# Optimization experiments

Measured on AMD Instinct MI355X. Metric: run time of the kernel, lower is better.

## Reference

```python
import jax, jax.numpy as jnp
import numpy as np

GAMMA = 2.5
K = 4
RHO = 0.085
TAU_CLIP = 5.0
NUM_HEADS = 8


def setup_inputs() -> dict:
    key = jax.random.key(0)
    ks = jax.random.split(key, 4)
    B, T, C = 2, 2048, 512
    x = jax.random.normal(ks[0], (B, T, C), jnp.float32)
    tau = jax.random.uniform(ks[1], (B, T, T), jnp.float32)
    s = 1.0 / np.sqrt(C)
    Wqkv = jax.random.normal(ks[2], (C, 3 * C), jnp.float32) * s
    bqkv = jnp.zeros((3 * C,), jnp.float32)
    Wproj = jax.random.normal(ks[3], (C, C), jnp.float32) * s
    bproj = jnp.zeros((C,), jnp.float32)
    return dict(x=x, tau=tau, Wqkv=Wqkv, bqkv=bqkv, Wproj=Wproj, bproj=bproj)


def reference(x, tau, Wqkv, bqkv, Wproj, bproj):
    B, T, C = x.shape
    H = NUM_HEADS
    D = C // H
    qkv = x @ Wqkv + bqkv                       # [B,T,3C]
    q, k, v = jnp.split(qkv, 3, axis=-1)
    q = q.reshape(B, T, H, D).transpose(0, 2, 1, 3)   # [B,H,T,D]
    k = k.reshape(B, T, H, D).transpose(0, 2, 1, 3)
    v = v.reshape(B, T, H, D).transpose(0, 2, 1, 3)
    scale = D ** -0.5
    logits = jnp.einsum('bhtd,bhsd->bhts', q, k) * scale   # [B,H,T,T]
    pheromone_bias = GAMMA * jnp.log(tau + 1e-8)           # [B,T,T]
    logits = logits + pheromone_bias[:, None]
    # top-K keys per query from tau define the sparse mask (LOCAL_WINDOW=0)
    k_val = min(K, T)
    idx = jax.lax.top_k(tau, k_val)[1]                     # [B,T,K]
    mask = jnp.zeros((B, T, T), bool).at[
        jnp.arange(B)[:, None, None], jnp.arange(T)[None, :, None], idx
    ].set(True)
    logits = jnp.where(mask[:, None], logits, -jnp.inf)
    attn = jax.nn.softmax(logits, axis=-1)                 # [B,H,T,T]
    # EMA pheromone (tau) update, no gradient in original (torch.no_grad)
    signal = attn.mean(axis=1)                             # [B,T,T]
    tau_new = (1.0 - RHO) * tau + signal ** 3
    tau_new = tau_new / (tau_new.sum(axis=-1, keepdims=True) + 1e-8)
    tau_new = jnp.minimum(tau_new, TAU_CLIP)
    tau_new = jax.lax.stop_gradient(tau_new)
    out = jnp.einsum('bhts,bhsd->bthd', attn, v).reshape(B, T, C)
    out = out @ Wproj + bproj
    return out, tau_new
```

## Files before the change

### kernel.cpp

```cpp
#include <hip/hip_runtime.h>
#include <hip/hip_bf16.h>
#include <math.h>

#define BB 2
#define TT 2048
#define CC 512
#define HH 8
#define DD 64
#define KK 4
#define C3 1536
#define MROWS (BB*TT)

#define G1_NT (C3/64)
#define G1_BLOCKS (G1_NT*(MROWS/128))
#define G2_NT (CC/64)
#define G2_BLOCKS (G2_NT*(MROWS/128))

typedef __attribute__((ext_vector_type(8))) short bf16x8;
typedef __attribute__((ext_vector_type(4))) float floatx4;

static __device__ __forceinline__ unsigned short f2bf(float f) {
  unsigned int u = __float_as_uint(f);
  return (unsigned short)((u + 0x7fffu + ((u >> 16) & 1u)) >> 16);
}
static __device__ __forceinline__ float bf2f(unsigned short u) {
  return __uint_as_float(((unsigned int)u) << 16);
}

template<bool BF16OUT>
static __device__ __forceinline__ void gemm_body(
    int bid, int nt,
    const unsigned short* __restrict__ A,
    const unsigned short* __restrict__ Bt,
    const float* __restrict__ bias,
    void* __restrict__ Cout, int N, int K) {
  __shared__ bf16x8 As[128 * 4];
  __shared__ bf16x8 Bs[64 * 4];
  const int tid  = threadIdx.x;
  const int wave = tid >> 6;
  const int lane = tid & 63;
  const int n0 = (bid % nt) * 64;
  const int m0 = (bid / nt) * 128;
  const int m_off = (wave >> 1) * 64;
  const int n_off = (wave & 1) * 32;
  const int lrow = lane >> 2;
  const int lx   = ((lane & 3) ^ ((lane >> 3) & 3)) * 8;
  const int fr = lane & 15;
  const int fq = lane >> 4;
  const int key = (fr >> 1) & 3;

  floatx4 acc[4][2];
#pragma unroll
  for (int i = 0; i < 4; ++i)
#pragma unroll
    for (int j = 0; j < 2; ++j) acc[i][j] = (floatx4){0.f, 0.f, 0.f, 0.f};

  for (int k0 = 0; k0 < K; k0 += 32) {
#pragma unroll
    for (int s = 0; s < 2; ++s) {
      int q = wave * 2 + s;
      const unsigned short* ga = A + (size_t)(m0 + q * 16 + lrow) * K + k0 + lx;
      __builtin_amdgcn_global_load_lds(
          (const __attribute__((address_space(1))) void*)ga,
          (__attribute__((address_space(3))) void*)((char*)As + q * 1024), 16, 0, 0);
    }
    const unsigned short* gb = Bt + (size_t)(n0 + wave * 16 + lrow) * K + k0 + lx;
    __builtin_amdgcn_global_load_lds(
        (const __attribute__((address_space(1))) void*)gb,
        (__attribute__((address_space(3))) void*)((char*)Bs + wave * 1024), 16, 0, 0);
    __syncthreads();
    bf16x8 a[4], b[2];
#pragma unroll
    for (int i = 0; i < 4; ++i)
      a[i] = As[(m_off + i * 16 + fr) * 4 + (fq ^ key)];
#pragma unroll
    for (int j = 0; j < 2; ++j)
      b[j] = Bs[(n_off + j * 16 + fr) * 4 + (fq ^ key)];
#pragma unroll
    for (int i = 0; i < 4; ++i)
#pragma unroll
      for (int j = 0; j < 2; ++j)
        acc[i][j] = __builtin_amdgcn_mfma_f32_16x16x32_bf16(a[i], b[j], acc[i][j], 0, 0, 0);
    __syncthreads();
  }
#pragma unroll
  for (int j = 0; j < 2; ++j) {
    int col = n0 + n_off + j * 16 + fr;
    float bv = bias[col];
#pragma unroll
    for (int i = 0; i < 4; ++i) {
#pragma unroll
      for (int r = 0; r < 4; ++r) {
        int row = m0 + m_off + i * 16 + fq * 4 + r;
        float v = acc[i][j][r] + bv;
        if (BF16OUT) ((unsigned short*)Cout)[(size_t)row * N + col] = f2bf(v);
        else         ((float*)Cout)[(size_t)row * N + col] = v;
      }
    }
  }
}

static __device__ __forceinline__ bool kv_better(float av, int ai, float bv, int bi) {
  return av > bv || (av == bv && ai < bi);
}
static __device__ __forceinline__ void kv_ce(float* v, int* i, int a, int b) {
  if (!kv_better(v[a], i[a], v[b], i[b])) {
    float tv = v[a]; v[a] = v[b]; v[b] = tv;
    int   ti = i[a]; i[a] = i[b]; i[b] = ti;
  }
}
static __device__ __forceinline__ void kv_merge(
    float* av, int* ai, const float* bv, const int* bi) {
  float cv[4]; int ci[4];
#pragma unroll
  for (int j = 0; j < 4; ++j) {
    bool t = kv_better(av[j], ai[j], bv[3 - j], bi[3 - j]);
    cv[j] = t ? av[j] : bv[3 - j];
    ci[j] = t ? ai[j] : bi[3 - j];
  }
  kv_ce(cv, ci, 0, 2); kv_ce(cv, ci, 1, 3);
  kv_ce(cv, ci, 0, 1); kv_ce(cv, ci, 2, 3);
#pragma unroll
  for (int j = 0; j < 4; ++j) { av[j] = cv[j]; ai[j] = ci[j]; }
}

static __device__ __forceinline__ void topk_body(
    int row, const float* __restrict__ tau, int* __restrict__ idx_out) {
  const int tid = threadIdx.x;
  const float4* rp = (const float4*)(tau + (size_t)row * TT);
  float4 f0 = rp[tid * 2], f1 = rp[tid * 2 + 1];
  float e[8] = { f0.x, f0.y, f0.z, f0.w, f1.x, f1.y, f1.z, f1.w };
  const int base = tid * 8;

  float tv[4] = { -1e30f, -1e30f, -1e30f, -1e30f };
  int   ti[4] = { 1 << 30, 1 << 30, 1 << 30, 1 << 30 };
#pragma unroll
  for (int k = 0; k < 8; ++k) {
    float v = e[k];
    if (v > tv[3]) {
      tv[3] = v; ti[3] = base + k;
      if (tv[3] > tv[2]) { float a=tv[2]; tv[2]=tv[3]; tv[3]=a; int b=ti[2]; ti[2]=ti[3]; ti[3]=b; }
      if (tv[2] > tv[1]) { float a=tv[1]; tv[1]=tv[2]; tv[2]=a; int b=ti[1]; ti[1]=ti[2]; ti[2]=b; }
      if (tv[1] > tv[0]) { float a=tv[0]; tv[0]=tv[1]; tv[1]=a; int b=ti[0]; ti[0]=ti[1]; ti[1]=b; }
    }
  }

#pragma unroll
  for (int step = 1; step <= 32; step <<= 1) {
    float bv[4]; int bi[4];
#pragma unroll
    for (int j = 0; j < 4; ++j) {
      bv[j] = __shfl_xor(tv[j], step, 64);
      bi[j] = __shfl_xor(ti[j], step, 64);
    }
    kv_merge(tv, ti, bv, bi);
  }

  __shared__ float swv[4][4];
  __shared__ int   swi[4][4];
  const int wave = tid >> 6, lane = tid & 63;
  if (lane == 0) {
#pragma unroll
    for (int j = 0; j < 4; ++j) { swv[wave][j] = tv[j]; swi[wave][j] = ti[j]; }
  }
  __syncthreads();
  if (tid == 0) {
    float m0[4], m1[4]; int x0[4], x1[4];
#pragma unroll
    for (int j = 0; j < 4; ++j) { m0[j] = swv[0][j]; x0[j] = swi[0][j]; }
#pragma unroll
    for (int j = 0; j < 4; ++j) { m1[j] = swv[1][j]; x1[j] = swi[1][j]; }
    kv_merge(m0, x0, m1, x1);
#pragma unroll
    for (int j = 0; j < 4; ++j) { m1[j] = swv[2][j]; x1[j] = swi[2][j]; }
    float m2[4]; int x2[4];
#pragma unroll
    for (int j = 0; j < 4; ++j) { m2[j] = swv[3][j]; x2[j] = swi[3][j]; }
    kv_merge(m1, x1, m2, x2);
    kv_merge(m0, x0, m1, x1);
    int4 w = { x0[0], x0[1], x0[2], x0[3] };
    *((int4*)(idx_out + row * KK)) = w;
  }
}

static __device__ __forceinline__ void transpose_body(
    int t, int nbx, const float* __restrict__ W, unsigned short* __restrict__ Wt,
    int R, int Cn) {
  __shared__ unsigned short tile[32][33];
  const int c0 = (t % nbx) * 32, r0 = (t / nbx) * 32;
  const int tx = threadIdx.x & 31, ty = threadIdx.x >> 5;
#pragma unroll
  for (int i = 0; i < 4; ++i) {
    int r = ty + i * 8;
    tile[r][tx] = f2bf(W[(size_t)(r0 + r) * Cn + c0 + tx]);
  }
  __syncthreads();
#pragma unroll
  for (int i = 0; i < 4; ++i) {
    int r = ty + i * 8;
    Wt[(size_t)(c0 + r) * R + r0 + tx] = tile[tx][r];
  }
}

__global__ __launch_bounds__(256) void prep_kernel(
    const float* __restrict__ x, unsigned short* __restrict__ x_bf,
    const float* __restrict__ Wqkv, unsigned short* __restrict__ wqkv_t,
    const float* __restrict__ Wproj, unsigned short* __restrict__ wproj_t) {
  const int bid = blockIdx.x;
  if (bid < 1024) {
    int g = bid * 256 + threadIdx.x;
    const float4* p = (const float4*)x;
    float4 f0 = p[g * 2], f1 = p[g * 2 + 1];
    union { unsigned short u[8]; uint4 v; } pk;
    pk.u[0]=f2bf(f0.x); pk.u[1]=f2bf(f0.y); pk.u[2]=f2bf(f0.z); pk.u[3]=f2bf(f0.w);
    pk.u[4]=f2bf(f1.x); pk.u[5]=f2bf(f1.y); pk.u[6]=f2bf(f1.z); pk.u[7]=f2bf(f1.w);
    ((uint4*)x_bf)[g] = pk.v;
  } else if (bid < 1024 + 768) {
    transpose_body(bid - 1024, C3 / 32, Wqkv, wqkv_t, CC, C3);
  } else {
    transpose_body(bid - 1792, CC / 32, Wproj, wproj_t, CC, CC);
  }
}

__global__ __launch_bounds__(256) void gemm1_topk_kernel(
    const unsigned short* __restrict__ x_bf,
    const unsigned short* __restrict__ wqkv_t,
    const float* __restrict__ bqkv, unsigned short* __restrict__ qkv_bf,
    const float* __restrict__ tau, int* __restrict__ idx_out) {
  if (blockIdx.x < G1_BLOCKS)
    gemm_body<true>(blockIdx.x, G1_NT, x_bf, wqkv_t, bqkv, qkv_bf, C3, CC);
  else
    topk_body(blockIdx.x - G1_BLOCKS, tau, idx_out);
}

__global__ __launch_bounds__(512) void attn_tau_kernel(
    const unsigned short* __restrict__ qkv, const float* __restrict__ tau,
    const int* __restrict__ idx_in, unsigned short* __restrict__ attn_bf,
    float* __restrict__ tau_out) {
  const int row  = blockIdx.x;
  const int b    = row >> 11;
  const int tid  = threadIdx.x;
  const int h    = tid >> 6;
  const int lane = tid & 63;

  __shared__ int   idx4[KK];
  __shared__ float tau4[KK];
  __shared__ float ps[HH][KK];
  __shared__ float s3s[KK];
  if (tid < KK) {
    int s = idx_in[row * KK + tid];
    idx4[tid] = s;
    tau4[tid] = tau[(size_t)row * TT + s];
  }
  const float4* rp = (const float4*)(tau + (size_t)row * TT);
  float4 tv4 = rp[tid];
  __syncthreads();

  const float q = bf2f(qkv[(size_t)row * C3 + h * DD + lane]);
  float kv[KK], vv[KK];
#pragma unroll
  for (int j = 0; j < KK; ++j) {
    size_t bs = ((size_t)(b * TT + idx4[j])) * C3 + h * DD + lane;
    kv[j] = bf2f(qkv[bs + CC]);
    vv[j] = bf2f(qkv[bs + 2 * CC]);
  }

  float p[KK];
#pragma unroll
  for (int j = 0; j < KK; ++j) p[j] = q * kv[j];
#pragma unroll
  for (int off = 32; off > 0; off >>= 1)
#pragma unroll
    for (int j = 0; j < KK; ++j) p[j] += __shfl_xor(p[j], off, 64);

  float logit[KK];
#pragma unroll
  for (int j = 0; j < KK; ++j)
    logit[j] = p[j] * 0.125f + 2.5f * logf(tau4[j] + 1e-8f);

  float m = fmaxf(fmaxf(logit[0], logit[1]), fmaxf(logit[2], logit[3]));
  float den = 0.f;
#pragma unroll
  for (int j = 0; j < KK; ++j) { p[j] = expf(logit[j] - m); den += p[j]; }
  float inv = 1.f / den;
#pragma unroll
  for (int j = 0; j < KK; ++j) p[j] *= inv;

  float o = 0.f;
#pragma unroll
  for (int j = 0; j < KK; ++j) o += p[j] * vv[j];
  attn_bf[(size_t)row * CC + h * DD + lane] = f2bf(o);

  if (lane < KK) ps[h][lane] = p[lane];
  __syncthreads();
  if (tid < KK) {
    float s = 0.f;
#pragma unroll
    for (int k = 0; k < HH; ++k) s += ps[k][tid];
    s *= (1.0f / HH);
    s3s[tid] = s * s * s;
  }
  __syncthreads();

  float v[4] = { tv4.x, tv4.y, tv4.z, tv4.w };
  int i4[KK]; float s3[KK];
#pragma unroll
  for (int j = 0; j < KK; ++j) { i4[j] = idx4[j]; s3[j] = s3s[j]; }
  const float keep = 1.0f - 0.085f;
  const int base = tid * 4;
  float local = 0.f;
#pragma unroll
  for (int i = 0; i < 4; ++i) {
    float t = keep * v[i];
#pragma unroll
    for (int j = 0; j < KK; ++j)
      if (base + i == i4[j]) t += s3[j];
    v[i] = t;
    local += t;
  }
#pragma unroll
  for (int off = 32; off > 0; off >>= 1) local += __shfl_xor(local, off, 64);
  __shared__ float wsum[HH];
  __shared__ float tot;
  if (lane == 0) wsum[h] = local;
  __syncthreads();
  if (tid == 0) {
    float s = 0.f;
#pragma unroll
    for (int k = 0; k < HH; ++k) s += wsum[k];
    tot = s;
  }
  __syncthreads();
  float invs = 1.f / (tot + 1e-8f);
  float4 o4 = { fminf(v[0]*invs,5.f), fminf(v[1]*invs,5.f),
                fminf(v[2]*invs,5.f), fminf(v[3]*invs,5.f) };
  ((float4*)(tau_out + (size_t)row * TT))[tid] = o4;
}

__global__ __launch_bounds__(256) void gemm2_kernel(
    const unsigned short* __restrict__ attn_bf,
    const unsigned short* __restrict__ wproj_t,
    const float* __restrict__ bproj, float* __restrict__ out) {
  gemm_body<false>(blockIdx.x, G2_NT, attn_bf, wproj_t, bproj, out, CC, CC);
}

extern "C" void kernel_launch(void* const* d_in, const int* in_sizes, int n_in,
                              void* d_out, int out_size, void* d_ws, size_t ws_size,
                              hipStream_t stream) {
  const float* x     = (const float*)d_in[0];
  const float* tau   = (const float*)d_in[1];
  const float* Wqkv  = (const float*)d_in[2];
  const float* bqkv  = (const float*)d_in[3];
  const float* Wproj = (const float*)d_in[4];
  const float* bproj = (const float*)d_in[5];

  float* out     = (float*)d_out;
  float* tau_new = out + (size_t)MROWS * CC;

  char* w = (char*)d_ws;
  unsigned short* qkv_bf  = (unsigned short*)w; w += (size_t)MROWS * C3 * 2;
  unsigned short* x_bf    = (unsigned short*)w; w += (size_t)MROWS * CC * 2;
  unsigned short* wqkv_t  = (unsigned short*)w; w += (size_t)C3 * CC * 2;
  unsigned short* wproj_t = (unsigned short*)w; w += (size_t)CC * CC * 2;
  unsigned short* attn_bf = (unsigned short*)w; w += (size_t)MROWS * CC * 2;
  int*   idx = (int*)w;

  prep_kernel<<<2048, 256, 0, stream>>>(x, x_bf, Wqkv, wqkv_t, Wproj, wproj_t);

  gemm1_topk_kernel<<<G1_BLOCKS + MROWS, 256, 0, stream>>>(
      x_bf, wqkv_t, bqkv, qkv_bf, tau, idx);

  attn_tau_kernel<<<MROWS, 512, 0, stream>>>(qkv_bf, tau, idx, attn_bf, tau_new);

  gemm2_kernel<<<G2_BLOCKS, 256, 0, stream>>>(attn_bf, wproj_t, bproj, out);
}
```

Measured before the change: 145.7 us.

## Fuse top-k selection into attention/tau row kernel to read tau once

Moves the per-row top-k over tau out of the gemm1 kernel and into the per-row attention/tau-update kernel, which now holds the tau row in registers for both top-k and the EMA normalization. This removes a second full read of tau and the index buffer round trip. The row kernel drops to 256 threads with each wave handling two heads, and top-k no longer overlaps with the QKV GEMM.

```diff
diff --git a/kernel.cpp b/kernel.cpp
--- a/kernel.cpp
+++ b/kernel.cpp
@@ -124,65 +124,6 @@
   for (int j = 0; j < 4; ++j) { av[j] = cv[j]; ai[j] = ci[j]; }
 }
 
-static __device__ __forceinline__ void topk_body(
-    int row, const float* __restrict__ tau, int* __restrict__ idx_out) {
-  const int tid = threadIdx.x;
-  const float4* rp = (const float4*)(tau + (size_t)row * TT);
-  float4 f0 = rp[tid * 2], f1 = rp[tid * 2 + 1];
-  float e[8] = { f0.x, f0.y, f0.z, f0.w, f1.x, f1.y, f1.z, f1.w };
-  const int base = tid * 8;
-
-  float tv[4] = { -1e30f, -1e30f, -1e30f, -1e30f };
-  int   ti[4] = { 1 << 30, 1 << 30, 1 << 30, 1 << 30 };
-#pragma unroll
-  for (int k = 0; k < 8; ++k) {
-    float v = e[k];
-    if (v > tv[3]) {
-      tv[3] = v; ti[3] = base + k;
-      if (tv[3] > tv[2]) { float a=tv[2]; tv[2]=tv[3]; tv[3]=a; int b=ti[2]; ti[2]=ti[3]; ti[3]=b; }
-      if (tv[2] > tv[1]) { float a=tv[1]; tv[1]=tv[2]; tv[2]=a; int b=ti[1]; ti[1]=ti[2]; ti[2]=b; }
-      if (tv[1] > tv[0]) { float a=tv[0]; tv[0]=tv[1]; tv[1]=a; int b=ti[0]; ti[0]=ti[1]; ti[1]=b; }
-    }
-  }
-
-#pragma unroll
-  for (int step = 1; step <= 32; step <<= 1) {
-    float bv[4]; int bi[4];
-#pragma unroll
-    for (int j = 0; j < 4; ++j) {
-      bv[j] = __shfl_xor(tv[j], step, 64);
-      bi[j] = __shfl_xor(ti[j], step, 64);
-    }
-    kv_merge(tv, ti, bv, bi);
-  }
-
-  __shared__ float swv[4][4];
-  __shared__ int   swi[4][4];
-  const int wave = tid >> 6, lane = tid & 63;
-  if (lane == 0) {
-#pragma unroll
-    for (int j = 0; j < 4; ++j) { swv[wave][j] = tv[j]; swi[wave][j] = ti[j]; }
-  }
-  __syncthreads();
-  if (tid == 0) {
-    float m0[4], m1[4]; int x0[4], x1[4];
-#pragma unroll
-    for (int j = 0; j < 4; ++j) { m0[j] = swv[0][j]; x0[j] = swi[0][j]; }
-#pragma unroll
-    for (int j = 0; j < 4; ++j) { m1[j] = swv[1][j]; x1[j] = swi[1][j]; }
-    kv_merge(m0, x0, m1, x1);
-#pragma unroll
-    for (int j = 0; j < 4; ++j) { m1[j] = swv[2][j]; x1[j] = swi[2][j]; }
-    float m2[4]; int x2[4];
-#pragma unroll
-    for (int j = 0; j < 4; ++j) { m2[j] = swv[3][j]; x2[j] = swi[3][j]; }
-    kv_merge(m1, x1, m2, x2);
-    kv_merge(m0, x0, m1, x1);
-    int4 w = { x0[0], x0[1], x0[2], x0[3] };
-    *((int4*)(idx_out + row * KK)) = w;
-  }
-}
-
 static __device__ __forceinline__ void transpose_body(
     int t, int nbx, const float* __restrict__ W, unsigned short* __restrict__ Wt,
     int R, int Cn) {
@@ -222,76 +163,121 @@
   }
 }
 
-__global__ __launch_bounds__(256) void gemm1_topk_kernel(
+__global__ __launch_bounds__(256) void gemm1_kernel(
     const unsigned short* __restrict__ x_bf,
     const unsigned short* __restrict__ wqkv_t,
-    const float* __restrict__ bqkv, unsigned short* __restrict__ qkv_bf,
-    const float* __restrict__ tau, int* __restrict__ idx_out) {
-  if (blockIdx.x < G1_BLOCKS)
-    gemm_body<true>(blockIdx.x, G1_NT, x_bf, wqkv_t, bqkv, qkv_bf, C3, CC);
-  else
-    topk_body(blockIdx.x - G1_BLOCKS, tau, idx_out);
-}
-
-__global__ __launch_bounds__(512) void attn_tau_kernel(
+    const float* __restrict__ bqkv, unsigned short* __restrict__ qkv_bf) {
+  gemm_body<true>(blockIdx.x, G1_NT, x_bf, wqkv_t, bqkv, qkv_bf, C3, CC);
+}
+
+__global__ __launch_bounds__(256) void row_kernel(
     const unsigned short* __restrict__ qkv, const float* __restrict__ tau,
-    const int* __restrict__ idx_in, unsigned short* __restrict__ attn_bf,
-    float* __restrict__ tau_out) {
+    unsigned short* __restrict__ attn_bf, float* __restrict__ tau_out) {
   const int row  = blockIdx.x;
   const int b    = row >> 11;
   const int tid  = threadIdx.x;
-  const int h    = tid >> 6;
+  const int wv   = tid >> 6;
   const int lane = tid & 63;
 
   __shared__ int   idx4[KK];
   __shared__ float tau4[KK];
   __shared__ float ps[HH][KK];
   __shared__ float s3s[KK];
-  if (tid < KK) {
-    int s = idx_in[row * KK + tid];
-    idx4[tid] = s;
-    tau4[tid] = tau[(size_t)row * TT + s];
-  }
+  __shared__ float swv[4][4];
+  __shared__ int   swi[4][4];
+  __shared__ float wsum[4];
+  __shared__ float tot;
+
   const float4* rp = (const float4*)(tau + (size_t)row * TT);
-  float4 tv4 = rp[tid];
-  __syncthreads();
-
-  const float q = bf2f(qkv[(size_t)row * C3 + h * DD + lane]);
-  float kv[KK], vv[KK];
-#pragma unroll
-  for (int j = 0; j < KK; ++j) {
-    size_t bs = ((size_t)(b * TT + idx4[j])) * C3 + h * DD + lane;
-    kv[j] = bf2f(qkv[bs + CC]);
-    vv[j] = bf2f(qkv[bs + 2 * CC]);
-  }
-
-  float p[KK];
-#pragma unroll
-  for (int j = 0; j < KK; ++j) p[j] = q * kv[j];
-#pragma unroll
-  for (int off = 32; off > 0; off >>= 1)
-#pragma unroll
-    for (int j = 0; j < KK; ++j) p[j] += __shfl_xor(p[j], off, 64);
-
-  float logit[KK];
-#pragma unroll
-  for (int j = 0; j < KK; ++j)
-    logit[j] = p[j] * 0.125f + 2.5f * logf(tau4[j] + 1e-8f);
-
-  float m = fmaxf(fmaxf(logit[0], logit[1]), fmaxf(logit[2], logit[3]));
-  float den = 0.f;
-#pragma unroll
-  for (int j = 0; j < KK; ++j) { p[j] = expf(logit[j] - m); den += p[j]; }
-  float inv = 1.f / den;
-#pragma unroll
-  for (int j = 0; j < KK; ++j) p[j] *= inv;
-
-  float o = 0.f;
-#pragma unroll
-  for (int j = 0; j < KK; ++j) o += p[j] * vv[j];
-  attn_bf[(size_t)row * CC + h * DD + lane] = f2bf(o);
-
-  if (lane < KK) ps[h][lane] = p[lane];
+  float4 f0 = rp[tid * 2], f1 = rp[tid * 2 + 1];
+  float e[8] = { f0.x, f0.y, f0.z, f0.w, f1.x, f1.y, f1.z, f1.w };
+  const int base = tid * 8;
+
+  float tv[4] = { -1e30f, -1e30f, -1e30f, -1e30f };
+  int   ti[4] = { 1 << 30, 1 << 30, 1 << 30, 1 << 30 };
+#pragma unroll
+  for (int k = 0; k < 8; ++k) {
+    float v = e[k];
+    if (v > tv[3]) {
+      tv[3] = v; ti[3] = base + k;
+      if (tv[3] > tv[2]) { float a=tv[2]; tv[2]=tv[3]; tv[3]=a; int c=ti[2]; ti[2]=ti[3]; ti[3]=c; }
+      if (tv[2] > tv[1]) { float a=tv[1]; tv[1]=tv[2]; tv[2]=a; int c=ti[1]; ti[1]=ti[2]; ti[2]=c; }
+      if (tv[1] > tv[0]) { float a=tv[0]; tv[0]=tv[1]; tv[1]=a; int c=ti[0]; ti[0]=ti[1]; ti[1]=c; }
+    }
+  }
+#pragma unroll
+  for (int step = 1; step <= 32; step <<= 1) {
+    float bv[4]; int bi[4];
+#pragma unroll
+    for (int j = 0; j < 4; ++j) {
+      bv[j] = __shfl_xor(tv[j], step, 64);
+      bi[j] = __shfl_xor(ti[j], step, 64);
+    }
+    kv_merge(tv, ti, bv, bi);
+  }
+  if (lane == 0) {
+#pragma unroll
+    for (int j = 0; j < 4; ++j) { swv[wv][j] = tv[j]; swi[wv][j] = ti[j]; }
+  }
+  __syncthreads();
+  if (tid == 0) {
+    float m0[4], m1[4]; int x0[4], x1[4];
+#pragma unroll
+    for (int j = 0; j < 4; ++j) { m0[j] = swv[0][j]; x0[j] = swi[0][j]; }
+#pragma unroll
+    for (int j = 0; j < 4; ++j) { m1[j] = swv[1][j]; x1[j] = swi[1][j]; }
+    kv_merge(m0, x0, m1, x1);
+#pragma unroll
+    for (int j = 0; j < 4; ++j) { m1[j] = swv[2][j]; x1[j] = swi[2][j]; }
+    float m2[4]; int x2[4];
+#pragma unroll
+    for (int j = 0; j < 4; ++j) { m2[j] = swv[3][j]; x2[j] = swi[3][j]; }
+    kv_merge(m1, x1, m2, x2);
+    kv_merge(m0, x0, m1, x1);
+#pragma unroll
+    for (int j = 0; j < 4; ++j) { idx4[j] = x0[j]; tau4[j] = m0[j]; }
+  }
+  __syncthreads();
+
+  int   i4[KK]; float t4[KK];
+#pragma unroll
+  for (int j = 0; j < KK; ++j) { i4[j] = idx4[j]; t4[j] = tau4[j]; }
+
+#pragma unroll
+  for (int hh = 0; hh < 2; ++hh) {
+    const int h = wv + hh * 4;
+    const float q = bf2f(qkv[(size_t)row * C3 + h * DD + lane]);
+    float kv[KK], vv[KK];
+#pragma unroll
+    for (int j = 0; j < KK; ++j) {
+      size_t bs = ((size_t)(b * TT + i4[j])) * C3 + h * DD + lane;
+      kv[j] = bf2f(qkv[bs + CC]);
+      vv[j] = bf2f(qkv[bs + 2 * CC]);
+    }
+    float p[KK];
+#pragma unroll
+    for (int j = 0; j < KK; ++j) p[j] = q * kv[j];
+#pragma unroll
+    for (int off = 32; off > 0; off >>= 1)
+#pragma unroll
+      for (int j = 0; j < KK; ++j) p[j] += __shfl_xor(p[j], off, 64);
+    float logit[KK];
+#pragma unroll
+    for (int j = 0; j < KK; ++j)
+      logit[j] = p[j] * 0.125f + 2.5f * logf(t4[j] + 1e-8f);
+    float m = fmaxf(fmaxf(logit[0], logit[1]), fmaxf(logit[2], logit[3]));
+    float den = 0.f;
+#pragma unroll
+    for (int j = 0; j < KK; ++j) { p[j] = expf(logit[j] - m); den += p[j]; }
+    float inv = 1.f / den;
+#pragma unroll
+    for (int j = 0; j < KK; ++j) p[j] *= inv;
+    float o = 0.f;
+#pragma unroll
+    for (int j = 0; j < KK; ++j) o += p[j] * vv[j];
+    attn_bf[(size_t)row * CC + h * DD + lane] = f2bf(o);
+    if (lane < KK) ps[h][lane] = p[lane];
+  }
   __syncthreads();
   if (tid < KK) {
     float s = 0.f;
@@ -302,39 +288,32 @@
   }
   __syncthreads();
 
-  float v[4] = { tv4.x, tv4.y, tv4.z, tv4.w };
-  int i4[KK]; float s3[KK];
-#pragma unroll
-  for (int j = 0; j < KK; ++j) { i4[j] = idx4[j]; s3[j] = s3s[j]; }
+  float s3[KK];
+#pragma unroll
+  for (int j = 0; j < KK; ++j) s3[j] = s3s[j];
   const float keep = 1.0f - 0.085f;
-  const int base = tid * 4;
   float local = 0.f;
 #pragma unroll
-  for (int i = 0; i < 4; ++i) {
-    float t = keep * v[i];
+  for (int i = 0; i < 8; ++i) {
+    float t = keep * e[i];
 #pragma unroll
     for (int j = 0; j < KK; ++j)
       if (base + i == i4[j]) t += s3[j];
-    v[i] = t;
+    e[i] = t;
     local += t;
   }
 #pragma unroll
   for (int off = 32; off > 0; off >>= 1) local += __shfl_xor(local, off, 64);
-  __shared__ float wsum[HH];
-  __shared__ float tot;
-  if (lane == 0) wsum[h] = local;
-  __syncthreads();
-  if (tid == 0) {
-    float s = 0.f;
-#pragma unroll
-    for (int k = 0; k < HH; ++k) s += wsum[k];
-    tot = s;
-  }
-  __syncthreads();
-  float invs = 1.f / (tot + 1e-8f);
-  float4 o4 = { fminf(v[0]*invs,5.f), fminf(v[1]*invs,5.f),
-                fminf(v[2]*invs,5.f), fminf(v[3]*invs,5.f) };
-  ((float4*)(tau_out + (size_t)row * TT))[tid] = o4;
+  if (lane == 0) wsum[wv] = local;
+  __syncthreads();
+  if (tid == 0) tot = wsum[0] + wsum[1] + wsum[2] + wsum[3];
+  __syncthreads();
+  float inv = 1.f / (tot + 1e-8f);
+  float4* op = (float4*)(tau_out + (size_t)row * TT);
+  float4 o0 = { fminf(e[0]*inv,5.f), fminf(e[1]*inv,5.f), fminf(e[2]*inv,5.f), fminf(e[3]*inv,5.f) };
+  float4 o1 = { fminf(e[4]*inv,5.f), fminf(e[5]*inv,5.f), fminf(e[6]*inv,5.f), fminf(e[7]*inv,5.f) };
+  op[tid * 2] = o0;
+  op[tid * 2 + 1] = o1;
 }
 
 __global__ __launch_bounds__(256) void gemm2_kernel(
@@ -362,15 +341,13 @@
   unsigned short* x_bf    = (unsigned short*)w; w += (size_t)MROWS * CC * 2;
   unsigned short* wqkv_t  = (unsigned short*)w; w += (size_t)C3 * CC * 2;
   unsigned short* wproj_t = (unsigned short*)w; w += (size_t)CC * CC * 2;
-  unsigned short* attn_bf = (unsigned short*)w; w += (size_t)MROWS * CC * 2;
-  int*   idx = (int*)w;
+  unsigned short* attn_bf = (unsigned short*)w;
 
   prep_kernel<<<2048, 256, 0, stream>>>(x, x_bf, Wqkv, wqkv_t, Wproj, wproj_t);
 
-  gemm1_topk_kernel<<<G1_BLOCKS + MROWS, 256, 0, stream>>>(
-      x_bf, wqkv_t, bqkv, qkv_bf, tau, idx);
-
-  attn_tau_kernel<<<MROWS, 512, 0, stream>>>(qkv_bf, tau, idx, attn_bf, tau_new);
+  gemm1_kernel<<<G1_BLOCKS, 256, 0, stream>>>(x_bf, wqkv_t, bqkv, qkv_bf);
+
+  row_kernel<<<MROWS, 256, 0, stream>>>(qkv_bf, tau, attn_bf, tau_new);
 
   gemm2_kernel<<<G2_BLOCKS, 256, 0, stream>>>(attn_bf, wproj_t, bproj, out);
 }
```

Result: no change. 146.5 us (+0.6%).
